# Kernel optimization log

Hardware: AMD Instinct MI355X
Metric: run time of the kernel (lower is better)

Reference implementation:

```python
import jax, jax.numpy as jnp
import numpy as np
import math

B, T, E, H = 4, 1024, 1024, 16
HD = E // H  # 64, even -> rope_dim == head_dim, no pass-through
SCALE = HD ** -0.5
PI = math.pi


def setup_inputs() -> dict:
    key = jax.random.key(0)
    ks = jax.random.split(key, 16)
    d = {}
    d["x_real"] = jax.random.normal(ks[0], (B, T, E), jnp.float32)
    d["x_imag"] = jax.random.normal(ks[1], (B, T, E), jnp.float32)
    d["lat"] = jax.random.uniform(ks[2], (B, T), jnp.float32) * 180.0
    d["lon"] = jax.random.uniform(ks[3], (B, T), jnp.float32) * 360.0
    i = 4
    for p in ("q", "k", "v", "o"):
        d[p + "_log_mag"] = jax.random.normal(ks[i], (E, E), jnp.float32) * 0.1; i += 1
        d[p + "_phase"] = jax.random.uniform(ks[i], (E, E), jnp.float32, minval=-PI, maxval=PI); i += 1
        d[p + "_bmag"] = jnp.zeros((E,), jnp.float32)
        d[p + "_bphase"] = jnp.zeros((E,), jnp.float32)
    d["dist_scale"] = jax.random.normal(ks[i], (H,), jnp.float32) * 0.1 - 0.5; i += 1
    d["dist_offset"] = jnp.zeros((H,), jnp.float32)
    return d


def _clinear(xr, xi, log_mag, phase, bmag, bphase):
    # Complex linear with magnitude-phase weights: W = exp(log_mag) * e^{i*phase}
    mag = jnp.exp(log_mag)
    wr = mag * jnp.cos(phase)
    wi = mag * jnp.sin(phase)
    r = xr @ wr.T - xi @ wi.T + bmag * jnp.cos(bphase)
    im = xr @ wi.T + xi @ wr.T + bmag * jnp.sin(bphase)
    return r, im


def _rotate_half(x):
    x1, x2 = jnp.split(x, 2, axis=-1)
    return jnp.concatenate([-x2, x1], axis=-1)


def _rope(xr, xi, cos_full, sin_full):
    # applied identically to real and imag parts (head_dim even -> full rope)
    r = xr * cos_full + _rotate_half(xr) * sin_full
    im = xi * cos_full + _rotate_half(xi) * sin_full
    return r, im


def _heads(x):  # [B,T,E] -> [B,H,T,HD]
    return x.reshape(B, T, H, HD).transpose(0, 2, 1, 3)


def _forward(x_real, x_imag, lat, lon,
             q_log_mag, q_phase, q_bmag, q_bphase,
             k_log_mag, k_phase, k_bmag, k_bphase,
             v_log_mag, v_phase, v_bmag, v_bphase,
             o_log_mag, o_phase, o_bmag, o_bphase,
             dist_scale, dist_offset):
    qr, qi = _clinear(x_real, x_imag, q_log_mag, q_phase, q_bmag, q_bphase)
    kr, ki = _clinear(x_real, x_imag, k_log_mag, k_phase, k_bmag, k_bphase)
    vr, vi = _clinear(x_real, x_imag, v_log_mag, v_phase, v_bmag, v_bphase)
    qr, qi, kr, ki, vr, vi = map(_heads, (qr, qi, kr, ki, vr, vi))

    # complex RoPE cache
    pos = jnp.arange(T, dtype=jnp.float32)
    inv_freq = 1.0 / (10000.0 ** (jnp.arange(0, HD, 2, dtype=jnp.float32) / HD))
    freqs = pos[:, None] * inv_freq[None, :]          # [T, HD/2]
    cos = jnp.cos(freqs); sin = jnp.sin(freqs)
    cos_full = jnp.concatenate([cos, cos], -1)[None, None]  # [1,1,T,HD]
    sin_full = jnp.concatenate([sin, sin], -1)[None, None]
    qr, qi = _rope(qr, qi, cos_full, sin_full)
    kr, ki = _rope(kr, ki, cos_full, sin_full)

    # Hermitian attention scores: Re(Q K^H) = Re(Q)Re(K)^T + Im(Q)Im(K)^T
    scores = (jnp.einsum('bhqd,bhkd->bhqk', qr, kr)
              + jnp.einsum('bhqd,bhkd->bhqk', qi, ki)) * SCALE

    # spatial attention bias via haversine distance
    lat_rad = (lat - 90.0) / 180.0 * PI
    lon_rad = lon / 360.0 * (2.0 * PI)
    lat1 = lat_rad[:, :, None]; lat2 = lat_rad[:, None, :]   # [B,T,1],[B,1,T]
    dlat = lat2 - lat1
    dlon = lon_rad[:, None, :] - lon_rad[:, :, None]
    a = jnp.sin(dlat / 2) ** 2 + jnp.cos(lat1) * jnp.cos(lat2) * jnp.sin(dlon / 2) ** 2
    dist_deg = 2.0 * jnp.arcsin(jnp.sqrt(jnp.clip(a, 0.0, 1.0))) * (180.0 / PI)
    log_dist = jnp.log1p(dist_deg)[:, None]                  # [B,1,T,T]
    bias = dist_scale[None, :, None, None] * log_dist + dist_offset[None, :, None, None]
    scores = scores + bias

    # causal mask (block_size == T)
    causal = jnp.tril(jnp.ones((T, T), dtype=bool))
    scores = jnp.where(causal[None, None], scores, jnp.float32(-1e9))
    attn = jax.nn.softmax(scores, axis=-1)

    # complex value aggregation: real attention weights times complex V
    or_ = jnp.einsum('bhqk,bhkd->bhqd', attn, vr)
    oi_ = jnp.einsum('bhqk,bhkd->bhqd', attn, vi)
    or_ = or_.transpose(0, 2, 1, 3).reshape(B, T, E)
    oi_ = oi_.transpose(0, 2, 1, 3).reshape(B, T, E)

    yr, yi = _clinear(or_, oi_, o_log_mag, o_phase, o_bmag, o_bphase)
    return jnp.stack([yr, yi])  # [2,B,T,E] (real, imag)


def reference(x_real, x_imag, lat, lon,
              q_log_mag, q_phase, q_bmag, q_bphase,
              k_log_mag, k_phase, k_bmag, k_bphase,
              v_log_mag, v_phase, v_bmag, v_bphase,
              o_log_mag, o_phase, o_bmag, o_bphase,
              dist_scale, dist_offset):
    return _forward(x_real, x_imag, lat, lon,
                    q_log_mag, q_phase, q_bmag, q_bphase,
                    k_log_mag, k_phase, k_bmag, k_bphase,
                    v_log_mag, v_phase, v_bmag, v_bphase,
                    o_log_mag, o_phase, o_bmag, o_bphase,
                    dist_scale, dist_offset)
```

## Files before the change

### kernel.cpp

```cpp
#include <hip/hip_runtime.h>
#include <math.h>

#define B_ 4
#define T_ 1024
#define E_ 1024
#define H_ 16
#define HD_ 64

constexpr float SCALE_ = 0.125f;
constexpr float PI_F = 3.14159265358979323846f;

constexpr size_t BTE = (size_t)B_ * T_ * E_;
constexpr size_t BTT = (size_t)B_ * T_ * T_;
constexpr int M_ = B_ * T_;
constexpr int KC_ = 2 * E_;

typedef __attribute__((ext_vector_type(8))) short bf16x8;
typedef __attribute__((ext_vector_type(4))) float f32x4;

__device__ __forceinline__ short f2bf(float f) {
    unsigned int u = __float_as_uint(f);
    unsigned int r = (u + 0x7fffu + ((u >> 16) & 1u)) >> 16;
    return (short)r;
}
__device__ __forceinline__ float bf2f(short s) {
    return __uint_as_float(((unsigned int)(unsigned short)s) << 16);
}
__device__ __forceinline__ void fsplit(float v, short& h, short& l) {
    short hh = f2bf(v);
    h = hh;
    l = f2bf(v - bf2f(hh));
}
__device__ __forceinline__ void gl_lds16(const void* g, void* l) {
    __builtin_amdgcn_global_load_lds(
        (const __attribute__((address_space(1))) unsigned int*)g,
        (__attribute__((address_space(3))) unsigned int*)l, 16, 0, 0);
}

__global__ __launch_bounds__(256) void wgen(const float* __restrict__ lm,
                                            const float* __restrict__ ph,
                                            short* __restrict__ W) {
    int idx = blockIdx.x * 256 + threadIdx.x;
    int n = idx >> 10, k = idx & 1023;
    float m = expf(lm[idx]);
    float s, c;
    sincosf(ph[idx], &s, &c);
    float wr = m * c, wi = m * s;
    size_t r0 = (size_t)n * KC_;
    size_t r1 = (size_t)(n + 1024) * KC_;
    W[r0 + k]        = f2bf(wr);
    W[r0 + 1024 + k] = f2bf(-wi);
    W[r1 + k]        = f2bf(wi);
    W[r1 + 1024 + k] = f2bf(wr);
}

__global__ __launch_bounds__(256) void wgen_split(const float* __restrict__ lm,
                                                  const float* __restrict__ ph,
                                                  short* __restrict__ Wh,
                                                  short* __restrict__ Wl) {
    int idx = blockIdx.x * 256 + threadIdx.x;
    int n = idx >> 10, k = idx & 1023;
    float m = expf(lm[idx]);
    float s, c;
    sincosf(ph[idx], &s, &c);
    float wr = m * c, wi = m * s;
    size_t o0 = (size_t)n * KC_ + k;
    size_t o1 = (size_t)n * KC_ + 1024 + k;
    size_t o2 = (size_t)(n + 1024) * KC_ + k;
    size_t o3 = (size_t)(n + 1024) * KC_ + 1024 + k;
    short h, l;
    fsplit(wr,  h, l); Wh[o0] = h; Wl[o0] = l;
    fsplit(-wi, h, l); Wh[o1] = h; Wl[o1] = l;
    fsplit(wi,  h, l); Wh[o2] = h; Wl[o2] = l;
    fsplit(wr,  h, l); Wh[o3] = h; Wl[o3] = l;
}

__global__ __launch_bounds__(256) void xcat_split(const float* __restrict__ xr,
                                                  const float* __restrict__ xi,
                                                  short* __restrict__ xh,
                                                  short* __restrict__ xl) {
    size_t idx = (size_t)blockIdx.x * 256 + threadIdx.x;
    size_t m = idx >> 10, k = idx & 1023;
    short h, l;
    fsplit(xr[idx], h, l);
    xh[m * KC_ + k] = h; xl[m * KC_ + k] = l;
    fsplit(xi[idx], h, l);
    xh[m * KC_ + 1024 + k] = h; xl[m * KC_ + 1024 + k] = l;
}

__global__ __launch_bounds__(256) void geodist(const float* __restrict__ lat,
                                               const float* __restrict__ lon,
                                               short* __restrict__ ld) {
    size_t idx = (size_t)blockIdx.x * 256 + threadIdx.x;
    int k = (int)(idx & (T_ - 1));
    int q = (int)((idx >> 10) & (T_ - 1));
    int b = (int)(idx >> 20);
    float la1 = (lat[b * T_ + q] - 90.f) * (PI_F / 180.f);
    float la2 = (lat[b * T_ + k] - 90.f) * (PI_F / 180.f);
    float lo1 = lon[b * T_ + q] * (PI_F / 180.f);
    float lo2 = lon[b * T_ + k] * (PI_F / 180.f);
    float sdla = sinf((la2 - la1) * 0.5f);
    float sdlo = sinf((lo2 - lo1) * 0.5f);
    float a = sdla * sdla + cosf(la1) * cosf(la2) * sdlo * sdlo;
    a = fminf(fmaxf(a, 0.f), 1.f);
    float dd = 2.f * asinf(sqrtf(a)) * (180.f / PI_F);
    ld[idx] = f2bf(log1pf(dd));
}

__global__ __launch_bounds__(256) void cgemm_qk(const short* __restrict__ Ah,
                                                const short* __restrict__ Al,
                                                const short* __restrict__ Wh,
                                                const short* __restrict__ Wl,
                                                const float* __restrict__ bmag,
                                                const float* __restrict__ bphase,
                                                short* __restrict__ Qh,
                                                short* __restrict__ Ql) {
    __shared__ short sAh[128 * 32], sAl[128 * 32];
    __shared__ short sBh[128 * 32], sBl[128 * 32];

    const int tid = threadIdx.x;
    const int w = tid >> 6, l = tid & 63;
    const int wm = w >> 1, wn = w & 1;
    const int wl = l & 15, g = l >> 4;

    int id = blockIdx.y * 32 + blockIdx.x;
    int swz = (id & 7) * 64 + (id >> 3);
    const int bm = (swz & 31) * 128;
    const int bn = (swz >> 5) * 128;

    f32x4 acc[4][4];
#pragma unroll
    for (int m = 0; m < 4; ++m)
#pragma unroll
        for (int n = 0; n < 4; ++n) acc[m][n] = (f32x4){0.f, 0.f, 0.f, 0.f};

    for (int k0 = 0; k0 < KC_; k0 += 32) {
        __syncthreads();
#pragma unroll
        for (int i = 0; i < 2; ++i) {
            int chunk = (w * 2 + i) * 64 + l;
            int row = chunk >> 2, kc = chunk & 3;
            size_t ga = (size_t)(bm + row) * KC_ + k0 + kc * 8;
            size_t gb = (size_t)(bn + row) * KC_ + k0 + kc * 8;
            gl_lds16(Ah + ga, sAh + (w * 2 + i) * 64 * 8);
            gl_lds16(Al + ga, sAl + (w * 2 + i) * 64 * 8);
            gl_lds16(Wh + gb, sBh + (w * 2 + i) * 64 * 8);
            gl_lds16(Wl + gb, sBl + (w * 2 + i) * 64 * 8);
        }
        __syncthreads();

        bf16x8 afh[4], afl[4], bfh[4], bfl[4];
#pragma unroll
        for (int m = 0; m < 4; ++m) {
            afh[m] = *(const bf16x8*)&sAh[(wm * 64 + m * 16 + wl) * 32 + g * 8];
            afl[m] = *(const bf16x8*)&sAl[(wm * 64 + m * 16 + wl) * 32 + g * 8];
        }
#pragma unroll
        for (int n = 0; n < 4; ++n) {
            bfh[n] = *(const bf16x8*)&sBh[(wn * 64 + n * 16 + wl) * 32 + g * 8];
            bfl[n] = *(const bf16x8*)&sBl[(wn * 64 + n * 16 + wl) * 32 + g * 8];
        }
#pragma unroll
        for (int m = 0; m < 4; ++m)
#pragma unroll
            for (int n = 0; n < 4; ++n) {
                acc[m][n] = __builtin_amdgcn_mfma_f32_16x16x32_bf16(afh[m], bfh[n], acc[m][n], 0, 0, 0);
                acc[m][n] = __builtin_amdgcn_mfma_f32_16x16x32_bf16(afh[m], bfl[n], acc[m][n], 0, 0, 0);
                acc[m][n] = __builtin_amdgcn_mfma_f32_16x16x32_bf16(afl[m], bfh[n], acc[m][n], 0, 0, 0);
            }
    }

#pragma unroll
    for (int n = 0; n < 4; ++n) {
        const int col = bn + wn * 64 + n * 16 + wl;
        const int ch = col & 1023;
        float sb, cb;
        sincosf(bphase[ch], &sb, &cb);
        const float bias = bmag[ch] * (col < 1024 ? cb : sb);
#pragma unroll
        for (int m = 0; m < 4; ++m)
#pragma unroll
            for (int r = 0; r < 4; ++r) acc[m][n][r] += bias;
    }

#pragma unroll
    for (int n = 0; n < 2; ++n) {
        const int j = n * 16 + wl;
        const float invf = expf(-(2.f * j / 64.f) * 9.210340371976184f);
#pragma unroll
        for (int m = 0; m < 4; ++m)
#pragma unroll
            for (int r = 0; r < 4; ++r) {
                const int row = bm + wm * 64 + m * 16 + g * 4 + r;
                const float th = (float)(row & 1023) * invf;
                float s_, c_;
                sincosf(th, &s_, &c_);
                const float x1 = acc[m][n][r], x2 = acc[m][n + 2][r];
                acc[m][n][r]     = x1 * c_ - x2 * s_;
                acc[m][n + 2][r] = x2 * c_ + x1 * s_;
            }
    }

#pragma unroll
    for (int n = 0; n < 4; ++n) {
        const int col = bn + wn * 64 + n * 16 + wl;
        const int ch = col & 1023;
        const int off = (ch >> 6) * 128 + (ch & 63) + ((col >= 1024) ? 64 : 0);
#pragma unroll
        for (int m = 0; m < 4; ++m)
#pragma unroll
            for (int r = 0; r < 4; ++r) {
                const int row = bm + wm * 64 + m * 16 + g * 4 + r;
                short h_, l_;
                fsplit(acc[m][n][r], h_, l_);
                Qh[(size_t)row * KC_ + off] = h_;
                Ql[(size_t)row * KC_ + off] = l_;
            }
    }
}

__global__ __launch_bounds__(256) void cgemm_mfma(const short* __restrict__ A,
                                                  const short* __restrict__ W,
                                                  const float* __restrict__ bmag,
                                                  const float* __restrict__ bphase,
                                                  short* __restrict__ outbf,
                                                  float* __restrict__ outr,
                                                  float* __restrict__ outi,
                                                  int mode) {
    __shared__ short sA[128 * 32];
    __shared__ short sB[128 * 32];

    const int tid = threadIdx.x;
    const int w = tid >> 6, l = tid & 63;
    const int wm = w >> 1, wn = w & 1;
    const int wl = l & 15, g = l >> 4;

    int id = blockIdx.y * 32 + blockIdx.x;
    int swz = (id & 7) * 64 + (id >> 3);
    const int bm = (swz & 31) * 128;
    const int bn = (swz >> 5) * 128;

    f32x4 acc[4][4];
#pragma unroll
    for (int m = 0; m < 4; ++m)
#pragma unroll
        for (int n = 0; n < 4; ++n) acc[m][n] = (f32x4){0.f, 0.f, 0.f, 0.f};

    for (int k0 = 0; k0 < KC_; k0 += 32) {
        __syncthreads();
#pragma unroll
        for (int i = 0; i < 2; ++i) {
            int chunk = (w * 2 + i) * 64 + l;
            int row = chunk >> 2, kc = chunk & 3;
            gl_lds16(A + (size_t)(bm + row) * KC_ + k0 + kc * 8, sA + (w * 2 + i) * 64 * 8);
            gl_lds16(W + (size_t)(bn + row) * KC_ + k0 + kc * 8, sB + (w * 2 + i) * 64 * 8);
        }
        __syncthreads();

        bf16x8 af[4], bfr[4];
#pragma unroll
        for (int m = 0; m < 4; ++m)
            af[m] = *(const bf16x8*)&sA[(wm * 64 + m * 16 + wl) * 32 + g * 8];
#pragma unroll
        for (int n = 0; n < 4; ++n)
            bfr[n] = *(const bf16x8*)&sB[(wn * 64 + n * 16 + wl) * 32 + g * 8];
#pragma unroll
        for (int m = 0; m < 4; ++m)
#pragma unroll
            for (int n = 0; n < 4; ++n)
                acc[m][n] = __builtin_amdgcn_mfma_f32_16x16x32_bf16(af[m], bfr[n], acc[m][n], 0, 0, 0);
    }

#pragma unroll
    for (int n = 0; n < 4; ++n) {
        const int col = bn + wn * 64 + n * 16 + wl;
        const int ch = col & 1023;
        float sb, cb;
        sincosf(bphase[ch], &sb, &cb);
        const float bias = bmag[ch] * (col < 1024 ? cb : sb);
#pragma unroll
        for (int m = 0; m < 4; ++m) {
#pragma unroll
            for (int r = 0; r < 4; ++r) {
                const int row = bm + wm * 64 + m * 16 + g * 4 + r;
                const float v = acc[m][n][r] + bias;
                if (mode == 0) {
                    const int hh = ch >> 6, d = ch & 63;
                    outbf[(size_t)row * KC_ + hh * 128 + d + ((col >= 1024) ? 64 : 0)] = f2bf(v);
                } else {
                    if (col < 1024) outr[(size_t)row * E_ + col] = v;
                    else            outi[(size_t)row * E_ + (col - 1024)] = v;
                }
            }
        }
    }
}

__global__ __launch_bounds__(512) void attn_split(const short* __restrict__ qh,
                                                  const short* __restrict__ ql,
                                                  const short* __restrict__ kh,
                                                  const short* __restrict__ kl,
                                                  const short* __restrict__ vc,
                                                  const short* __restrict__ ldb,
                                                  const float* __restrict__ dsc,
                                                  const float* __restrict__ dof,
                                                  short* __restrict__ otc) {
    __shared__ short sKh[64 * 128];
    __shared__ short sKl[64 * 128];
    __shared__ short sV[2][64 * 66];
    __shared__ short sP[8][16 * 68];

    const int j = blockIdx.x;
    const int h = j & 15;
    const int idx = j >> 4;
    const int b = idx & 3;
    const int q4 = idx >> 2;
    const int qt = (q4 < 4) ? (7 - q4) : (q4 - 4);

    const int tid = threadIdx.x;
    const int w = tid >> 6, l = tid & 63;
    const int wl = l & 15, g = l >> 4;

    const float dsch = dsc[h], dofh = dof[h];

    bf16x8 aqh[4], aql[4];
    {
        const size_t qbase = ((size_t)(b * T_) + qt * 128 + w * 16 + wl) * KC_ + h * 128;
#pragma unroll
        for (int ks = 0; ks < 4; ++ks) {
            aqh[ks] = *(const bf16x8*)(qh + qbase + ks * 32 + g * 8);
            aql[ks] = *(const bf16x8*)(ql + qbase + ks * 32 + g * 8);
        }
    }

    f32x4 accR[4], accI[4];
#pragma unroll
    for (int nb = 0; nb < 4; ++nb) {
        accR[nb] = (f32x4){0.f, 0.f, 0.f, 0.f};
        accI[nb] = (f32x4){0.f, 0.f, 0.f, 0.f};
    }
    float m_run[4], l_run[4];
#pragma unroll
    for (int r = 0; r < 4; ++r) { m_run[r] = -3.0e38f; l_run[r] = 0.f; }

    const int nkt = 2 * qt + 2;
    for (int kt = 0; kt < nkt; ++kt) {
        __syncthreads();

#pragma unroll
        for (int i = 0; i < 2; ++i) {
            int chunk = (w * 2 + i) * 64 + l;
            int row = chunk >> 4;
            int c8 = (chunk & 15) ^ ((row & 7) << 1);
            size_t src = ((size_t)(b * T_) + kt * 64 + row) * KC_ + h * 128 + c8 * 8;
            gl_lds16(kh + src, sKh + (w * 2 + i) * 64 * 8);
            gl_lds16(kl + src, sKl + (w * 2 + i) * 64 * 8);
        }
        {
            const short* vrow = vc + ((size_t)(b * T_) + kt * 64 + l) * KC_ + h * 128;
            const int comp = w >> 2;
            const int d0 = (w & 3) * 16;
#pragma unroll
            for (int half = 0; half < 2; ++half) {
                bf16x8 v8 = *(const bf16x8*)(vrow + comp * 64 + d0 + half * 8);
#pragma unroll
                for (int jj = 0; jj < 8; ++jj) sV[comp][(d0 + half * 8 + jj) * 66 + l] = v8[jj];
            }
        }
        __syncthreads();

        f32x4 s[4];
#pragma unroll
        for (int nb = 0; nb < 4; ++nb) s[nb] = (f32x4){0.f, 0.f, 0.f, 0.f};
#pragma unroll
        for (int nb = 0; nb < 4; ++nb) {
            const int ktl = nb * 16 + wl;
#pragma unroll
            for (int ks = 0; ks < 4; ++ks) {
                const int pc8 = (ks * 4 + g) ^ ((ktl & 7) << 1);
                const bf16x8 bkh = *(const bf16x8*)&sKh[ktl * 128 + pc8 * 8];
                const bf16x8 bkl = *(const bf16x8*)&sKl[ktl * 128 + pc8 * 8];
                s[nb] = __builtin_amdgcn_mfma_f32_16x16x32_bf16(aqh[ks], bkh, s[nb], 0, 0, 0);
                s[nb] = __builtin_amdgcn_mfma_f32_16x16x32_bf16(aqh[ks], bkl, s[nb], 0, 0, 0);
                s[nb] = __builtin_amdgcn_mfma_f32_16x16x32_bf16(aql[ks], bkh, s[nb], 0, 0, 0);
            }
        }

        const int qg0 = qt * 128 + w * 16 + g * 4;
        const int kg0 = kt * 64;
        const bool domask = (kt >= 2 * qt);
#pragma unroll
        for (int nb = 0; nb < 4; ++nb) {
            const int kg = kg0 + nb * 16 + wl;
            const short* ldp = ldb + ((size_t)b * T_ + qg0) * T_ + kg;
#pragma unroll
            for (int r = 0; r < 4; ++r) {
                float sv = s[nb][r] * SCALE_ + dsch * bf2f(ldp[(size_t)r * T_]) + dofh;
                if (domask && kg > qg0 + r) sv = -1.0e9f;
                s[nb][r] = sv;
            }
        }

#pragma unroll
        for (int r = 0; r < 4; ++r) {
            float mt = fmaxf(fmaxf(s[0][r], s[1][r]), fmaxf(s[2][r], s[3][r]));
            mt = fmaxf(mt, __shfl_xor(mt, 1));
            mt = fmaxf(mt, __shfl_xor(mt, 2));
            mt = fmaxf(mt, __shfl_xor(mt, 4));
            mt = fmaxf(mt, __shfl_xor(mt, 8));
            const float mnew = fmaxf(m_run[r], mt);
            const float sc = __expf(m_run[r] - mnew);
            m_run[r] = mnew;
            float rs = 0.f;
#pragma unroll
            for (int nb = 0; nb < 4; ++nb) {
                const float p = __expf(s[nb][r] - mnew);
                s[nb][r] = p;
                rs += p;
            }
            rs += __shfl_xor(rs, 1);
            rs += __shfl_xor(rs, 2);
            rs += __shfl_xor(rs, 4);
            rs += __shfl_xor(rs, 8);
            l_run[r] = l_run[r] * sc + rs;
#pragma unroll
            for (int nb = 0; nb < 4; ++nb) { accR[nb][r] *= sc; accI[nb][r] *= sc; }
        }

#pragma unroll
        for (int nb = 0; nb < 4; ++nb)
#pragma unroll
            for (int r = 0; r < 4; ++r)
                sP[w][(g * 4 + r) * 68 + nb * 16 + wl] = f2bf(s[nb][r]);

        bf16x8 ap[2];
#pragma unroll
        for (int ks = 0; ks < 2; ++ks)
            ap[ks] = *(const bf16x8*)&sP[w][wl * 68 + ks * 32 + g * 8];
#pragma unroll
        for (int nb = 0; nb < 4; ++nb) {
#pragma unroll
            for (int ks = 0; ks < 2; ++ks) {
                const bf16x8 bvr = *(const bf16x8*)&sV[0][(nb * 16 + wl) * 66 + ks * 32 + g * 8];
                const bf16x8 bvi = *(const bf16x8*)&sV[1][(nb * 16 + wl) * 66 + ks * 32 + g * 8];
                accR[nb] = __builtin_amdgcn_mfma_f32_16x16x32_bf16(ap[ks], bvr, accR[nb], 0, 0, 0);
                accI[nb] = __builtin_amdgcn_mfma_f32_16x16x32_bf16(ap[ks], bvi, accI[nb], 0, 0, 0);
            }
        }
    }

    float inv[4];
#pragma unroll
    for (int r = 0; r < 4; ++r) inv[r] = 1.0f / l_run[r];
#pragma unroll
    for (int nb = 0; nb < 4; ++nb) {
#pragma unroll
        for (int r = 0; r < 4; ++r) {
            const int q = qt * 128 + w * 16 + g * 4 + r;
            const int d = nb * 16 + wl;
            const size_t base = ((size_t)(b * T_) + q) * KC_ + h * 64 + d;
            otc[base] = f2bf(accR[nb][r] * inv[r]);
            otc[base + 1024] = f2bf(accI[nb][r] * inv[r]);
        }
    }
}

extern "C" void kernel_launch(void* const* d_in, const int* in_sizes, int n_in,
                              void* d_out, int out_size, void* d_ws, size_t ws_size,
                              hipStream_t stream) {
    const float* x_r  = (const float*)d_in[0];
    const float* x_i  = (const float*)d_in[1];
    const float* lat  = (const float*)d_in[2];
    const float* lon  = (const float*)d_in[3];
    const float* q_lm = (const float*)d_in[4];
    const float* q_ph = (const float*)d_in[5];
    const float* q_bm = (const float*)d_in[6];
    const float* q_bp = (const float*)d_in[7];
    const float* k_lm = (const float*)d_in[8];
    const float* k_ph = (const float*)d_in[9];
    const float* k_bm = (const float*)d_in[10];
    const float* k_bp = (const float*)d_in[11];
    const float* v_lm = (const float*)d_in[12];
    const float* v_ph = (const float*)d_in[13];
    const float* v_bm = (const float*)d_in[14];
    const float* v_bp = (const float*)d_in[15];
    const float* o_lm = (const float*)d_in[16];
    const float* o_ph = (const float*)d_in[17];
    const float* o_bm = (const float*)d_in[18];
    const float* o_bp = (const float*)d_in[19];
    const float* dsc  = (const float*)d_in[20];
    const float* dof  = (const float*)d_in[21];

    char* ws = (char*)d_ws;
    const size_t MB = 1024u * 1024u;
    short* Wv  = (short*)(ws + 0 * MB);
    short* Wo  = (short*)(ws + 8 * MB);
    short* Wqh = (short*)(ws + 16 * MB);
    short* Wql = (short*)(ws + 24 * MB);
    short* Wkh = (short*)(ws + 32 * MB);
    short* Wkl = (short*)(ws + 40 * MB);
    short* xch = (short*)(ws + 48 * MB);
    short* xcl = (short*)(ws + 64 * MB);
    short* qhh = (short*)(ws + 80 * MB);
    short* qll = (short*)(ws + 96 * MB);
    short* khh = (short*)(ws + 112 * MB);
    short* kll = (short*)(ws + 128 * MB);
    short* vcb = (short*)(ws + 144 * MB);
    short* otc = (short*)(ws + 160 * MB);
    short* ldt = (short*)(ws + 176 * MB);

    wgen_split<<<(E_ * E_) / 256, 256, 0, stream>>>(q_lm, q_ph, Wqh, Wql);
    wgen_split<<<(E_ * E_) / 256, 256, 0, stream>>>(k_lm, k_ph, Wkh, Wkl);
    wgen<<<(E_ * E_) / 256, 256, 0, stream>>>(v_lm, v_ph, Wv);
    wgen<<<(E_ * E_) / 256, 256, 0, stream>>>(o_lm, o_ph, Wo);
    xcat_split<<<BTE / 256, 256, 0, stream>>>(x_r, x_i, xch, xcl);
    geodist<<<BTT / 256, 256, 0, stream>>>(lat, lon, ldt);

    dim3 ggrid(M_ / 128, KC_ / 128);
    cgemm_qk<<<ggrid, 256, 0, stream>>>(xch, xcl, Wqh, Wql, q_bm, q_bp, qhh, qll);
    cgemm_qk<<<ggrid, 256, 0, stream>>>(xch, xcl, Wkh, Wkl, k_bm, k_bp, khh, kll);
    cgemm_mfma<<<ggrid, 256, 0, stream>>>(xch, Wv, v_bm, v_bp, vcb, nullptr, nullptr, 0);

    attn_split<<<512, 512, 0, stream>>>(qhh, qll, khh, kll, vcb, ldt, dsc, dof, otc);

    float* yr = (float*)d_out;
    float* yi = (float*)d_out + BTE;
    cgemm_mfma<<<ggrid, 256, 0, stream>>>(otc, Wo, o_bm, o_bp, nullptr, yr, yi, 1);
}
```

Baseline: 649.3 us.

## Fuse Q and K projection GEMMs and XOR-swizzle LDS tiles to avoid bank conflicts

Merges the two separate Q and K split-bf16 complex GEMM launches into one kernel that loads each A tile once and accumulates both Q and K outputs. This halves the A-operand global and LDS traffic for those projections. It also switches the LDS layouts of the QK and V/O GEMMs, and of the K tiles in attention, to an XOR-swizzled interleaved form to reduce bank conflicts. The cost is doubled accumulator registers in the fused kernel (128 fp32 per thread), which may lower occupancy or cause spills.

```diff
diff --git a/kernel.cpp b/kernel.cpp
--- a/kernel.cpp
+++ b/kernel.cpp
@@ -107,16 +107,23 @@
     ld[idx] = f2bf(log1pf(dd));
 }
 
-__global__ __launch_bounds__(256) void cgemm_qk(const short* __restrict__ Ah,
-                                                const short* __restrict__ Al,
-                                                const short* __restrict__ Wh,
-                                                const short* __restrict__ Wl,
-                                                const float* __restrict__ bmag,
-                                                const float* __restrict__ bphase,
-                                                short* __restrict__ Qh,
-                                                short* __restrict__ Ql) {
-    __shared__ short sAh[128 * 32], sAl[128 * 32];
-    __shared__ short sBh[128 * 32], sBl[128 * 32];
+__global__ __launch_bounds__(256) void cgemm_qk2(const short* __restrict__ Ah,
+                                                 const short* __restrict__ Al,
+                                                 const short* __restrict__ Qwh,
+                                                 const short* __restrict__ Qwl,
+                                                 const short* __restrict__ Kwh,
+                                                 const short* __restrict__ Kwl,
+                                                 const float* __restrict__ qbm,
+                                                 const float* __restrict__ qbp,
+                                                 const float* __restrict__ kbm,
+                                                 const float* __restrict__ kbp,
+                                                 short* __restrict__ Qh,
+                                                 short* __restrict__ Ql,
+                                                 short* __restrict__ Kh,
+                                                 short* __restrict__ Kl) {
+    __shared__ short sA[128 * 64];
+    __shared__ short sQ[128 * 64];
+    __shared__ short sK[128 * 64];
 
     const int tid = threadIdx.x;
     const int w = tid >> 6, l = tid & 63;
@@ -128,59 +135,74 @@
     const int bm = (swz & 31) * 128;
     const int bn = (swz >> 5) * 128;
 
-    f32x4 acc[4][4];
+    f32x4 accQ[4][4], accK[4][4];
 #pragma unroll
     for (int m = 0; m < 4; ++m)
 #pragma unroll
-        for (int n = 0; n < 4; ++n) acc[m][n] = (f32x4){0.f, 0.f, 0.f, 0.f};
+        for (int n = 0; n < 4; ++n) {
+            accQ[m][n] = (f32x4){0.f, 0.f, 0.f, 0.f};
+            accK[m][n] = (f32x4){0.f, 0.f, 0.f, 0.f};
+        }
 
     for (int k0 = 0; k0 < KC_; k0 += 32) {
         __syncthreads();
 #pragma unroll
-        for (int i = 0; i < 2; ++i) {
-            int chunk = (w * 2 + i) * 64 + l;
-            int row = chunk >> 2, kc = chunk & 3;
-            size_t ga = (size_t)(bm + row) * KC_ + k0 + kc * 8;
-            size_t gb = (size_t)(bn + row) * KC_ + k0 + kc * 8;
-            gl_lds16(Ah + ga, sAh + (w * 2 + i) * 64 * 8);
-            gl_lds16(Al + ga, sAl + (w * 2 + i) * 64 * 8);
-            gl_lds16(Wh + gb, sBh + (w * 2 + i) * 64 * 8);
-            gl_lds16(Wl + gb, sBl + (w * 2 + i) * 64 * 8);
+        for (int i = 0; i < 4; ++i) {
+            const int chunk = (w * 4 + i) * 64 + l;
+            const int row = chunk >> 3;
+            const int c8 = (chunk & 7) ^ (row & 7);
+            const size_t ca = (size_t)(bm + row) * KC_ + k0 + (c8 & 3) * 8;
+            const size_t cb = (size_t)(bn + row) * KC_ + k0 + (c8 & 3) * 8;
+            gl_lds16(((c8 < 4) ? Ah : Al) + ca, sA + (size_t)(w * 4 + i) * 64 * 8);
+            gl_lds16(((c8 < 4) ? Qwh : Qwl) + cb, sQ + (size_t)(w * 4 + i) * 64 * 8);
+            gl_lds16(((c8 < 4) ? Kwh : Kwl) + cb, sK + (size_t)(w * 4 + i) * 64 * 8);
         }
         __syncthreads();
 
-        bf16x8 afh[4], afl[4], bfh[4], bfl[4];
+        bf16x8 afh[4], afl[4];
 #pragma unroll
         for (int m = 0; m < 4; ++m) {
-            afh[m] = *(const bf16x8*)&sAh[(wm * 64 + m * 16 + wl) * 32 + g * 8];
-            afl[m] = *(const bf16x8*)&sAl[(wm * 64 + m * 16 + wl) * 32 + g * 8];
+            const int ra = wm * 64 + m * 16 + wl;
+            const int sw = ra & 7;
+            afh[m] = *(const bf16x8*)&sA[(ra * 8 + (g ^ sw)) * 8];
+            afl[m] = *(const bf16x8*)&sA[(ra * 8 + ((g + 4) ^ sw)) * 8];
         }
 #pragma unroll
         for (int n = 0; n < 4; ++n) {
-            bfh[n] = *(const bf16x8*)&sBh[(wn * 64 + n * 16 + wl) * 32 + g * 8];
-            bfl[n] = *(const bf16x8*)&sBl[(wn * 64 + n * 16 + wl) * 32 + g * 8];
-        }
-#pragma unroll
-        for (int m = 0; m < 4; ++m)
-#pragma unroll
-            for (int n = 0; n < 4; ++n) {
-                acc[m][n] = __builtin_amdgcn_mfma_f32_16x16x32_bf16(afh[m], bfh[n], acc[m][n], 0, 0, 0);
-                acc[m][n] = __builtin_amdgcn_mfma_f32_16x16x32_bf16(afh[m], bfl[n], acc[m][n], 0, 0, 0);
-                acc[m][n] = __builtin_amdgcn_mfma_f32_16x16x32_bf16(afl[m], bfh[n], acc[m][n], 0, 0, 0);
-            }
+            const int rb = wn * 64 + n * 16 + wl;
+            const int sw = rb & 7;
+            const bf16x8 qh_ = *(const bf16x8*)&sQ[(rb * 8 + (g ^ sw)) * 8];
+            const bf16x8 ql_ = *(const bf16x8*)&sQ[(rb * 8 + ((g + 4) ^ sw)) * 8];
+            const bf16x8 kh_ = *(const bf16x8*)&sK[(rb * 8 + (g ^ sw)) * 8];
+            const bf16x8 kl_ = *(const bf16x8*)&sK[(rb * 8 + ((g + 4) ^ sw)) * 8];
+#pragma unroll
+            for (int m = 0; m < 4; ++m) {
+                accQ[m][n] = __builtin_amdgcn_mfma_f32_16x16x32_bf16(afh[m], qh_, accQ[m][n], 0, 0, 0);
+                accQ[m][n] = __builtin_amdgcn_mfma_f32_16x16x32_bf16(afh[m], ql_, accQ[m][n], 0, 0, 0);
+                accQ[m][n] = __builtin_amdgcn_mfma_f32_16x16x32_bf16(afl[m], qh_, accQ[m][n], 0, 0, 0);
+                accK[m][n] = __builtin_amdgcn_mfma_f32_16x16x32_bf16(afh[m], kh_, accK[m][n], 0, 0, 0);
+                accK[m][n] = __builtin_amdgcn_mfma_f32_16x16x32_bf16(afh[m], kl_, accK[m][n], 0, 0, 0);
+                accK[m][n] = __builtin_amdgcn_mfma_f32_16x16x32_bf16(afl[m], kh_, accK[m][n], 0, 0, 0);
+            }
+        }
     }
 
 #pragma unroll
     for (int n = 0; n < 4; ++n) {
         const int col = bn + wn * 64 + n * 16 + wl;
         const int ch = col & 1023;
-        float sb, cb;
-        sincosf(bphase[ch], &sb, &cb);
-        const float bias = bmag[ch] * (col < 1024 ? cb : sb);
+        float qs, qc, ks, kc;
+        sincosf(qbp[ch], &qs, &qc);
+        sincosf(kbp[ch], &ks, &kc);
+        const float qbias = qbm[ch] * (col < 1024 ? qc : qs);
+        const float kbias = kbm[ch] * (col < 1024 ? kc : ks);
 #pragma unroll
         for (int m = 0; m < 4; ++m)
 #pragma unroll
-            for (int r = 0; r < 4; ++r) acc[m][n][r] += bias;
+            for (int r = 0; r < 4; ++r) {
+                accQ[m][n][r] += qbias;
+                accK[m][n][r] += kbias;
+            }
     }
 
 #pragma unroll
@@ -195,9 +217,12 @@
                 const float th = (float)(row & 1023) * invf;
                 float s_, c_;
                 sincosf(th, &s_, &c_);
-                const float x1 = acc[m][n][r], x2 = acc[m][n + 2][r];
-                acc[m][n][r]     = x1 * c_ - x2 * s_;
-                acc[m][n + 2][r] = x2 * c_ + x1 * s_;
+                float x1 = accQ[m][n][r], x2 = accQ[m][n + 2][r];
+                accQ[m][n][r]     = x1 * c_ - x2 * s_;
+                accQ[m][n + 2][r] = x2 * c_ + x1 * s_;
+                x1 = accK[m][n][r]; x2 = accK[m][n + 2][r];
+                accK[m][n][r]     = x1 * c_ - x2 * s_;
+                accK[m][n + 2][r] = x2 * c_ + x1 * s_;
             }
     }
 
@@ -212,9 +237,12 @@
             for (int r = 0; r < 4; ++r) {
                 const int row = bm + wm * 64 + m * 16 + g * 4 + r;
                 short h_, l_;
-                fsplit(acc[m][n][r], h_, l_);
+                fsplit(accQ[m][n][r], h_, l_);
                 Qh[(size_t)row * KC_ + off] = h_;
                 Ql[(size_t)row * KC_ + off] = l_;
+                fsplit(accK[m][n][r], h_, l_);
+                Kh[(size_t)row * KC_ + off] = h_;
+                Kl[(size_t)row * KC_ + off] = l_;
             }
     }
 }
@@ -227,8 +255,7 @@
                                                   float* __restrict__ outr,
                                                   float* __restrict__ outi,
                                                   int mode) {
-    __shared__ short sA[128 * 32];
-    __shared__ short sB[128 * 32];
+    __shared__ short sAB[128 * 64];
 
     const int tid = threadIdx.x;
     const int w = tid >> 6, l = tid & 63;
@@ -249,21 +276,28 @@
     for (int k0 = 0; k0 < KC_; k0 += 32) {
         __syncthreads();
 #pragma unroll
-        for (int i = 0; i < 2; ++i) {
-            int chunk = (w * 2 + i) * 64 + l;
-            int row = chunk >> 2, kc = chunk & 3;
-            gl_lds16(A + (size_t)(bm + row) * KC_ + k0 + kc * 8, sA + (w * 2 + i) * 64 * 8);
-            gl_lds16(W + (size_t)(bn + row) * KC_ + k0 + kc * 8, sB + (w * 2 + i) * 64 * 8);
+        for (int i = 0; i < 4; ++i) {
+            const int chunk = (w * 4 + i) * 64 + l;
+            const int row = chunk >> 3;
+            const int c8 = (chunk & 7) ^ (row & 7);
+            const short* src = (c8 < 4)
+                ? A + (size_t)(bm + row) * KC_ + k0 + (c8 & 3) * 8
+                : W + (size_t)(bn + row) * KC_ + k0 + (c8 & 3) * 8;
+            gl_lds16(src, sAB + (size_t)(w * 4 + i) * 64 * 8);
         }
         __syncthreads();
 
         bf16x8 af[4], bfr[4];
 #pragma unroll
-        for (int m = 0; m < 4; ++m)
-            af[m] = *(const bf16x8*)&sA[(wm * 64 + m * 16 + wl) * 32 + g * 8];
-#pragma unroll
-        for (int n = 0; n < 4; ++n)
-            bfr[n] = *(const bf16x8*)&sB[(wn * 64 + n * 16 + wl) * 32 + g * 8];
+        for (int m = 0; m < 4; ++m) {
+            const int ra = wm * 64 + m * 16 + wl;
+            af[m] = *(const bf16x8*)&sAB[(ra * 8 + (g ^ (ra & 7))) * 8];
+        }
+#pragma unroll
+        for (int n = 0; n < 4; ++n) {
+            const int rb = wn * 64 + n * 16 + wl;
+            bfr[n] = *(const bf16x8*)&sAB[(rb * 8 + ((g + 4) ^ (rb & 7))) * 8];
+        }
 #pragma unroll
         for (int m = 0; m < 4; ++m)
 #pragma unroll
@@ -351,7 +385,7 @@
         for (int i = 0; i < 2; ++i) {
             int chunk = (w * 2 + i) * 64 + l;
             int row = chunk >> 4;
-            int c8 = (chunk & 15) ^ ((row & 7) << 1);
+            int c8 = (chunk & 15) ^ (row & 15);
             size_t src = ((size_t)(b * T_) + kt * 64 + row) * KC_ + h * 128 + c8 * 8;
             gl_lds16(kh + src, sKh + (w * 2 + i) * 64 * 8);
             gl_lds16(kl + src, sKl + (w * 2 + i) * 64 * 8);
@@ -377,7 +411,7 @@
             const int ktl = nb * 16 + wl;
 #pragma unroll
             for (int ks = 0; ks < 4; ++ks) {
-                const int pc8 = (ks * 4 + g) ^ ((ktl & 7) << 1);
+                const int pc8 = (ks * 4 + g) ^ (ktl & 15);
                 const bf16x8 bkh = *(const bf16x8*)&sKh[ktl * 128 + pc8 * 8];
                 const bf16x8 bkl = *(const bf16x8*)&sKl[ktl * 128 + pc8 * 8];
                 s[nb] = __builtin_amdgcn_mfma_f32_16x16x32_bf16(aqh[ks], bkh, s[nb], 0, 0, 0);
@@ -517,8 +551,9 @@
     geodist<<<BTT / 256, 256, 0, stream>>>(lat, lon, ldt);
 
     dim3 ggrid(M_ / 128, KC_ / 128);
-    cgemm_qk<<<ggrid, 256, 0, stream>>>(xch, xcl, Wqh, Wql, q_bm, q_bp, qhh, qll);
-    cgemm_qk<<<ggrid, 256, 0, stream>>>(xch, xcl, Wkh, Wkl, k_bm, k_bp, khh, kll);
+    cgemm_qk2<<<ggrid, 256, 0, stream>>>(xch, xcl, Wqh, Wql, Wkh, Wkl,
+                                         q_bm, q_bp, k_bm, k_bp,
+                                         qhh, qll, khh, kll);
     cgemm_mfma<<<ggrid, 256, 0, stream>>>(xch, Wv, v_bm, v_bp, vcb, nullptr, nullptr, 0);
 
     attn_split<<<512, 512, 0, stream>>>(qhh, qll, khh, kll, vcb, ldt, dsc, dof, otc);
```

Measured after the change: 601.8 us. 7.3% less time.
